# Kernel tuning notes

Measured on AMD Instinct MI355X. Metric: run time of the kernel, lower is better.

## Reference

```python
import jax, jax.numpy as jnp
import numpy as np

N_BLOCKS, B0, B1 = 128, 8, 8
OUT = N_BLOCKS * B0   # 1024
IN = N_BLOCKS * B1    # 1024 (cond_dim = None)
BATCH = 16384


def _masks():
    # block_diag_mask / block_tril_mask from flowjax (structural int32 constants)
    diag = np.zeros((OUT, IN), np.int32)
    tril = np.zeros((OUT, IN), np.int32)
    for i in range(N_BLOCKS):
        diag[i * B0:(i + 1) * B0, i * B1:(i + 1) * B1] = 1
        tril[(i + 1) * B0:, i * B1:(i + 1) * B1] = 1
    return jnp.asarray(diag), jnp.asarray(tril)


def setup_inputs() -> dict:
    key = jax.random.key(0)
    kx, kw, kb, ks = jax.random.split(key, 4)
    b_diag_mask, b_tril_mask = _masks()
    limit = float(np.sqrt(6.0 / (OUT + IN)))  # glorot_uniform
    W = jax.random.uniform(kw, (OUT, IN), jnp.float32, -limit, limit) * (b_diag_mask + b_tril_mask)
    bias = (jax.random.uniform(kb, (OUT,), jnp.float32) - 0.5) * (2.0 / np.sqrt(OUT))
    W_log_scale = jnp.log(jax.random.uniform(ks, (OUT, 1), jnp.float32, 1e-3, 1.0))
    x = jax.random.normal(kx, (BATCH, IN), jnp.float32)
    return {"x": x, "W": W, "bias": bias, "W_log_scale": W_log_scale,
            "b_diag_mask": b_diag_mask, "b_tril_mask": b_tril_mask}


def reference(x, W, bias, W_log_scale, b_diag_mask, b_tril_mask):
    # weight normalisation: exp() on diag blocks, identity on strictly-lower blocks,
    # per-row L2 norm, then learned scale
    Wm = jnp.exp(W) * b_diag_mask + W * b_tril_mask            # [OUT, IN]
    W_norms = jnp.linalg.norm(Wm, axis=-1, keepdims=True)      # [OUT, 1]
    Wn = jnp.exp(W_log_scale) * Wm / W_norms                   # [OUT, IN]
    # batched block-triangular matvec (vmap of W @ x + bias over batch)
    y = x @ Wn.T + bias                                        # [BATCH, OUT]
    # gather diagonal blocks -> (n_blocks, B0, B1), same row-major order as
    # jnp.where(b_diag_mask) indexing in the original
    idx = jnp.arange(N_BLOCKS)
    jac_3d = Wn.reshape(N_BLOCKS, B0, N_BLOCKS, B1)[idx, :, idx, :]  # [N_BLOCKS, B0, B1]
    return y, jnp.log(jac_3d)
```

## Files before the change

kernel.cpp:

```cpp
#include <hip/hip_runtime.h>

#define IN_DIM   1024
#define OUT_DIM  1024
#define BATCH    16384

#define BM 128
#define BN 128
#define BK 32

typedef __attribute__((ext_vector_type(8))) short          bf16x8;
typedef __attribute__((ext_vector_type(8))) unsigned short u16x8;
typedef __attribute__((ext_vector_type(4))) unsigned short u16x4;
typedef __attribute__((ext_vector_type(4))) float          f32x4;

__device__ __forceinline__ unsigned short f2bf(float f) {
    unsigned u = __float_as_uint(f);
    u += 0x7FFFu + ((u >> 16) & 1u);
    return (unsigned short)(u >> 16);
}
__device__ __forceinline__ float bf2f(unsigned short h) {
    return __uint_as_float((unsigned)h << 16);
}

#define GLOAD_LDS16(g, l)                                                      \
    __builtin_amdgcn_global_load_lds(                                          \
        (const __attribute__((address_space(1))) unsigned int*)(g),            \
        (__attribute__((address_space(3))) unsigned int*)(l), 16, 0, 0)

__global__ __launch_bounds__(256) void prep_kernel(
    const float* __restrict__ W, const float* __restrict__ wls,
    unsigned short* __restrict__ wh, unsigned short* __restrict__ wl,
    float* __restrict__ jac)
{
    const int warp = threadIdx.x >> 6;
    const int lane = threadIdx.x & 63;
    const int row  = blockIdx.x * 4 + warp;
    const int r    = row >> 3;
    const int d0   = r * 8;
    const int nk   = d0 + 8;
    const float* Wr = W + (size_t)row * IN_DIM;

    float ss = 0.f;
    for (int k = lane * 4; k < nk; k += 256) {
        float4 v = *(const float4*)&Wr[k];
        if (k >= d0) { v.x = expf(v.x); v.y = expf(v.y); v.z = expf(v.z); v.w = expf(v.w); }
        ss += v.x * v.x + v.y * v.y + v.z * v.z + v.w * v.w;
    }
    #pragma unroll
    for (int off = 32; off >= 1; off >>= 1) ss += __shfl_xor(ss, off);

    const float lscale = wls[row] - 0.5f * logf(ss);
    const float scale  = expf(lscale);

    for (int k = lane * 4; k < IN_DIM; k += 256) {
        float4 v = {0.f, 0.f, 0.f, 0.f};
        if (k < nk) {
            v = *(const float4*)&Wr[k];
            if (k >= d0) { v.x = expf(v.x); v.y = expf(v.y); v.z = expf(v.z); v.w = expf(v.w); }
            v.x *= scale; v.y *= scale; v.z *= scale; v.w *= scale;
        }
        u16x4 h, l;
        const float f[4] = {v.x, v.y, v.z, v.w};
        #pragma unroll
        for (int i = 0; i < 4; ++i) {
            h[i] = f2bf(f[i]);
            l[i] = f2bf(f[i] - bf2f(h[i]));
        }
        *(u16x4*)&wh[(size_t)row * IN_DIM + k] = h;
        *(u16x4*)&wl[(size_t)row * IN_DIM + k] = l;
    }
    if (lane < 8) jac[r * 64 + (row & 7) * 8 + lane] = lscale + Wr[d0 + lane];
}

__global__ __launch_bounds__(256, 2) void gemm_kernel(
    const float* __restrict__ x,
    const unsigned short* __restrict__ wh, const unsigned short* __restrict__ wl,
    const float* __restrict__ bias, float* __restrict__ y)
{
    __shared__ __align__(16) unsigned short smem[32768];

    const int bid = (int)blockIdx.x;
    const int seg = bid >> 7;
    const int sb  = bid & 127;
    const int nt  = 7 - seg;
    const int mt  = (sb & 7) * 16 + (sb >> 3);
    const int m0  = mt * BM;
    const int n0  = nt * BN;
    const int nsteps = (n0 + BN) >> 5;

    const int t    = threadIdx.x;
    const int lane = t & 63;
    const int wid  = t >> 6;
    const int wr   = wid >> 1;
    const int wc   = wid & 1;
    const int lr   = lane & 15;
    const int lq   = lane >> 4;

    const int mA = ((t >> 6) & 3) * 16 + (t & 15);
    const int kA = ((t >> 4) & 3) * 8;
    const float* xg = x + (size_t)(m0 + mA) * IN_DIM + kA;

    const unsigned short* whg = wh + (size_t)(n0 + wid * 32 + lr) * IN_DIM + lq * 8;
    const unsigned short* wlg = wl + (size_t)(n0 + wid * 32 + lr) * IN_DIM + lq * 8;

    f32x4 acc[4][4];
    #pragma unroll
    for (int i = 0; i < 4; ++i)
        #pragma unroll
        for (int j = 0; j < 4; ++j) acc[i][j] = (f32x4){0.f, 0.f, 0.f, 0.f};

    float4 xva, xvb, xvc, xvd;

    auto LOAD_X = [&](int k0) {
        xva = *(const float4*)(xg + k0);
        xvb = *(const float4*)(xg + k0 + 4);
        xvc = *(const float4*)(xg + 64 * IN_DIM + k0);
        xvd = *(const float4*)(xg + 64 * IN_DIM + k0 + 4);
    };
    auto STAGE_W = [&](int b, int k0) {
        unsigned short* whp = smem + b * 16384 + 8192  + wid * 1024;
        unsigned short* wlp = smem + b * 16384 + 12288 + wid * 1024;
        GLOAD_LDS16(whg + k0,                whp);
        GLOAD_LDS16(whg + k0 + 16 * IN_DIM,  whp + 512);
        GLOAD_LDS16(wlg + k0,                wlp);
        GLOAD_LDS16(wlg + k0 + 16 * IN_DIM,  wlp + 512);
    };
    auto CVT_X = [&](int b) {
        unsigned short* xhp = smem + b * 16384;
        unsigned short* xlp = xhp + 4096;
        const float fa[8] = {xva.x, xva.y, xva.z, xva.w, xvb.x, xvb.y, xvb.z, xvb.w};
        const float fb[8] = {xvc.x, xvc.y, xvc.z, xvc.w, xvd.x, xvd.y, xvd.z, xvd.w};
        u16x8 h0, l0, h1, l1;
        #pragma unroll
        for (int i = 0; i < 8; ++i) {
            h0[i] = f2bf(fa[i]);  l0[i] = f2bf(fa[i] - bf2f(h0[i]));
            h1[i] = f2bf(fb[i]);  l1[i] = f2bf(fb[i] - bf2f(h1[i]));
        }
        *(u16x8*)&xhp[t * 8]        = h0;
        *(u16x8*)&xlp[t * 8]        = l0;
        *(u16x8*)&xhp[2048 + t * 8] = h1;
        *(u16x8*)&xlp[2048 + t * 8] = l1;
    };
    auto COMPUTE = [&](int b) {
        const unsigned short* xh_ = smem + b * 16384;
        const unsigned short* xl_ = xh_ + 4096;
        const unsigned short* wh_ = xh_ + 8192;
        const unsigned short* wl_ = xh_ + 12288;
        const int ao = wr * 2048 + lane * 8;
        const int bo = wc * 2048 + lane * 8;
        bf16x8 bh[4], bl[4];
        #pragma unroll
        for (int fc = 0; fc < 4; ++fc) {
            bh[fc] = *(const bf16x8*)&wh_[bo + fc * 512];
            bl[fc] = *(const bf16x8*)&wl_[bo + fc * 512];
        }
        #pragma unroll
        for (int fr = 0; fr < 4; ++fr) {
            const bf16x8 ah = *(const bf16x8*)&xh_[ao + fr * 512];
            const bf16x8 al = *(const bf16x8*)&xl_[ao + fr * 512];
            #pragma unroll
            for (int fc = 0; fc < 4; ++fc) {
                acc[fr][fc] = __builtin_amdgcn_mfma_f32_16x16x32_bf16(ah, bh[fc], acc[fr][fc], 0, 0, 0);
                acc[fr][fc] = __builtin_amdgcn_mfma_f32_16x16x32_bf16(ah, bl[fc], acc[fr][fc], 0, 0, 0);
                acc[fr][fc] = __builtin_amdgcn_mfma_f32_16x16x32_bf16(al, bh[fc], acc[fr][fc], 0, 0, 0);
            }
        }
    };

    LOAD_X(0);
    STAGE_W(0, 0);
    CVT_X(0);
    __syncthreads();

    int buf = 0;
    int k0 = 0;
    for (int i = 0; i < nsteps; ++i, k0 += BK) {
        const bool has1 = (i + 1) < nsteps;
        if (has1) {
            LOAD_X(k0 + BK);
            STAGE_W(buf ^ 1, k0 + BK);
        }
        COMPUTE(buf);
        if (has1) CVT_X(buf ^ 1);
        __syncthreads();
        buf ^= 1;
    }

    float* yt = (float*)smem;
    const int er = t >> 2;
    const int ec = (t & 3) * 4;
    #pragma unroll
    for (int h = 0; h < 2; ++h) {
        if (wr == h) {
            #pragma unroll
            for (int fr = 0; fr < 4; ++fr) {
                const int row0 = fr * 16 + lq * 4;
                #pragma unroll
                for (int fc = 0; fc < 4; ++fc) {
                    const int col = wc * 64 + fc * 16 + lr;
                    #pragma unroll
                    for (int i = 0; i < 4; ++i)
                        yt[(row0 + i) * 132 + col] = acc[fr][fc][i];
                }
            }
        }
        __syncthreads();
        #pragma unroll
        for (int j = 0; j < 8; ++j) {
            const int col = ec + j * 16;
            float4 v = *(const float4*)&yt[er * 132 + col];
            const float4 bb = *(const float4*)&bias[n0 + col];
            v.x += bb.x; v.y += bb.y; v.z += bb.z; v.w += bb.w;
            *(float4*)&y[(size_t)(m0 + h * 64 + er) * OUT_DIM + n0 + col] = v;
        }
        __syncthreads();
    }
}

extern "C" void kernel_launch(void* const* d_in, const int* in_sizes, int n_in,
                              void* d_out, int out_size, void* d_ws, size_t ws_size,
                              hipStream_t stream)
{
    const float* x    = (const float*)d_in[0];
    const float* W    = (const float*)d_in[1];
    const float* bias = (const float*)d_in[2];
    const float* wls  = (const float*)d_in[3];

    unsigned short* wh = (unsigned short*)d_ws;
    unsigned short* wl = wh + (size_t)OUT_DIM * IN_DIM;
    float* y   = (float*)d_out;
    float* jac = y + (size_t)BATCH * OUT_DIM;

    prep_kernel<<<OUT_DIM / 4, 256, 0, stream>>>(W, wls, wh, wl, jac);

    gemm_kernel<<<8 * 128, 256, 0, stream>>>(x, wh, wl, bias, y);
}
```

Baseline: 191.9 us.

## Switch GEMM to single fp16 MFMA and widen N tile to 256

Replaces the bf16 hi/lo split (three MFMAs per tile) with a single fp16 conversion and one fp16 MFMA per fragment, and stores only one fp16 weight copy. The N tile grows to 256 with 512-thread blocks, halving the number of passes over x. This removes most matrix-core work and some memory traffic, at the cost of lower numerical accuracy (fp16 inputs without error compensation) and possible overflow or precision issues.

```diff
diff --git a/kernel.cpp b/kernel.cpp
--- a/kernel.cpp
+++ b/kernel.cpp
@@ -5,21 +5,16 @@
 #define BATCH    16384
 
 #define BM 128
-#define BN 128
+#define BN 256
 #define BK 32
 
-typedef __attribute__((ext_vector_type(8))) short          bf16x8;
-typedef __attribute__((ext_vector_type(8))) unsigned short u16x8;
+typedef __attribute__((ext_vector_type(8))) _Float16       f16x8;
 typedef __attribute__((ext_vector_type(4))) unsigned short u16x4;
 typedef __attribute__((ext_vector_type(4))) float          f32x4;
 
-__device__ __forceinline__ unsigned short f2bf(float f) {
-    unsigned u = __float_as_uint(f);
-    u += 0x7FFFu + ((u >> 16) & 1u);
-    return (unsigned short)(u >> 16);
-}
-__device__ __forceinline__ float bf2f(unsigned short h) {
-    return __uint_as_float((unsigned)h << 16);
+__device__ __forceinline__ unsigned short f2h(float f) {
+    _Float16 h = (_Float16)f;
+    return __builtin_bit_cast(unsigned short, h);
 }
 
 #define GLOAD_LDS16(g, l)                                                      \
@@ -29,8 +24,7 @@
 
 __global__ __launch_bounds__(256) void prep_kernel(
     const float* __restrict__ W, const float* __restrict__ wls,
-    unsigned short* __restrict__ wh, unsigned short* __restrict__ wl,
-    float* __restrict__ jac)
+    unsigned short* __restrict__ wf, float* __restrict__ jac)
 {
     const int warp = threadIdx.x >> 6;
     const int lane = threadIdx.x & 63;
@@ -59,30 +53,23 @@
             if (k >= d0) { v.x = expf(v.x); v.y = expf(v.y); v.z = expf(v.z); v.w = expf(v.w); }
             v.x *= scale; v.y *= scale; v.z *= scale; v.w *= scale;
         }
-        u16x4 h, l;
-        const float f[4] = {v.x, v.y, v.z, v.w};
-        #pragma unroll
-        for (int i = 0; i < 4; ++i) {
-            h[i] = f2bf(f[i]);
-            l[i] = f2bf(f[i] - bf2f(h[i]));
-        }
-        *(u16x4*)&wh[(size_t)row * IN_DIM + k] = h;
-        *(u16x4*)&wl[(size_t)row * IN_DIM + k] = l;
+        u16x4 h;
+        h[0] = f2h(v.x); h[1] = f2h(v.y); h[2] = f2h(v.z); h[3] = f2h(v.w);
+        *(u16x4*)&wf[(size_t)row * IN_DIM + k] = h;
     }
     if (lane < 8) jac[r * 64 + (row & 7) * 8 + lane] = lscale + Wr[d0 + lane];
 }
 
-__global__ __launch_bounds__(256, 2) void gemm_kernel(
-    const float* __restrict__ x,
-    const unsigned short* __restrict__ wh, const unsigned short* __restrict__ wl,
+__global__ __launch_bounds__(512, 2) void gemm_kernel(
+    const float* __restrict__ x, const unsigned short* __restrict__ wf,
     const float* __restrict__ bias, float* __restrict__ y)
 {
-    __shared__ __align__(16) unsigned short smem[32768];
+    __shared__ __align__(16) unsigned short smem[24576];
 
     const int bid = (int)blockIdx.x;
     const int seg = bid >> 7;
     const int sb  = bid & 127;
-    const int nt  = 7 - seg;
+    const int nt  = 3 - seg;
     const int mt  = (sb & 7) * 16 + (sb >> 3);
     const int m0  = mt * BM;
     const int n0  = nt * BN;
@@ -91,17 +78,16 @@
     const int t    = threadIdx.x;
     const int lane = t & 63;
     const int wid  = t >> 6;
-    const int wr   = wid >> 1;
-    const int wc   = wid & 1;
+    const int wr   = wid >> 2;
+    const int wc   = wid & 3;
     const int lr   = lane & 15;
     const int lq   = lane >> 4;
 
-    const int mA = ((t >> 6) & 3) * 16 + (t & 15);
+    const int mA = (t >> 6) * 16 + (t & 15);
     const int kA = ((t >> 4) & 3) * 8;
     const float* xg = x + (size_t)(m0 + mA) * IN_DIM + kA;
 
-    const unsigned short* whg = wh + (size_t)(n0 + wid * 32 + lr) * IN_DIM + lq * 8;
-    const unsigned short* wlg = wl + (size_t)(n0 + wid * 32 + lr) * IN_DIM + lq * 8;
+    const unsigned short* wg = wf + (size_t)(n0 + wid * 32 + lr) * IN_DIM + lq * 8;
 
     f32x4 acc[4][4];
     #pragma unroll
@@ -109,61 +95,40 @@
         #pragma unroll
         for (int j = 0; j < 4; ++j) acc[i][j] = (f32x4){0.f, 0.f, 0.f, 0.f};
 
-    float4 xva, xvb, xvc, xvd;
+    float4 xva, xvb;
 
     auto LOAD_X = [&](int k0) {
         xva = *(const float4*)(xg + k0);
         xvb = *(const float4*)(xg + k0 + 4);
-        xvc = *(const float4*)(xg + 64 * IN_DIM + k0);
-        xvd = *(const float4*)(xg + 64 * IN_DIM + k0 + 4);
     };
     auto STAGE_W = [&](int b, int k0) {
-        unsigned short* whp = smem + b * 16384 + 8192  + wid * 1024;
-        unsigned short* wlp = smem + b * 16384 + 12288 + wid * 1024;
-        GLOAD_LDS16(whg + k0,                whp);
-        GLOAD_LDS16(whg + k0 + 16 * IN_DIM,  whp + 512);
-        GLOAD_LDS16(wlg + k0,                wlp);
-        GLOAD_LDS16(wlg + k0 + 16 * IN_DIM,  wlp + 512);
+        unsigned short* wp = smem + b * 12288 + 4096 + wid * 1024;
+        GLOAD_LDS16(wg + k0,               wp);
+        GLOAD_LDS16(wg + k0 + 16 * IN_DIM, wp + 512);
     };
     auto CVT_X = [&](int b) {
-        unsigned short* xhp = smem + b * 16384;
-        unsigned short* xlp = xhp + 4096;
-        const float fa[8] = {xva.x, xva.y, xva.z, xva.w, xvb.x, xvb.y, xvb.z, xvb.w};
-        const float fb[8] = {xvc.x, xvc.y, xvc.z, xvc.w, xvd.x, xvd.y, xvd.z, xvd.w};
-        u16x8 h0, l0, h1, l1;
-        #pragma unroll
-        for (int i = 0; i < 8; ++i) {
-            h0[i] = f2bf(fa[i]);  l0[i] = f2bf(fa[i] - bf2f(h0[i]));
-            h1[i] = f2bf(fb[i]);  l1[i] = f2bf(fb[i] - bf2f(h1[i]));
-        }
-        *(u16x8*)&xhp[t * 8]        = h0;
-        *(u16x8*)&xlp[t * 8]        = l0;
-        *(u16x8*)&xhp[2048 + t * 8] = h1;
-        *(u16x8*)&xlp[2048 + t * 8] = l1;
+        unsigned short* xp = smem + b * 12288;
+        const float f[8] = {xva.x, xva.y, xva.z, xva.w, xvb.x, xvb.y, xvb.z, xvb.w};
+        f16x8 h;
+        #pragma unroll
+        for (int i = 0; i < 8; ++i) h[i] = (_Float16)f[i];
+        *(f16x8*)&xp[t * 8] = h;
     };
     auto COMPUTE = [&](int b) {
-        const unsigned short* xh_ = smem + b * 16384;
-        const unsigned short* xl_ = xh_ + 4096;
-        const unsigned short* wh_ = xh_ + 8192;
-        const unsigned short* wl_ = xh_ + 12288;
+        const unsigned short* xp = smem + b * 12288;
+        const unsigned short* wp = xp + 4096;
         const int ao = wr * 2048 + lane * 8;
         const int bo = wc * 2048 + lane * 8;
-        bf16x8 bh[4], bl[4];
-        #pragma unroll
-        for (int fc = 0; fc < 4; ++fc) {
-            bh[fc] = *(const bf16x8*)&wh_[bo + fc * 512];
-            bl[fc] = *(const bf16x8*)&wl_[bo + fc * 512];
-        }
+        f16x8 bfr[4];
+        #pragma unroll
+        for (int fc = 0; fc < 4; ++fc)
+            bfr[fc] = *(const f16x8*)&wp[bo + fc * 512];
         #pragma unroll
         for (int fr = 0; fr < 4; ++fr) {
-            const bf16x8 ah = *(const bf16x8*)&xh_[ao + fr * 512];
-            const bf16x8 al = *(const bf16x8*)&xl_[ao + fr * 512];
+            const f16x8 a = *(const f16x8*)&xp[ao + fr * 512];
             #pragma unroll
-            for (int fc = 0; fc < 4; ++fc) {
-                acc[fr][fc] = __builtin_amdgcn_mfma_f32_16x16x32_bf16(ah, bh[fc], acc[fr][fc], 0, 0, 0);
-                acc[fr][fc] = __builtin_amdgcn_mfma_f32_16x16x32_bf16(ah, bl[fc], acc[fr][fc], 0, 0, 0);
-                acc[fr][fc] = __builtin_amdgcn_mfma_f32_16x16x32_bf16(al, bh[fc], acc[fr][fc], 0, 0, 0);
-            }
+            for (int fc = 0; fc < 4; ++fc)
+                acc[fr][fc] = __builtin_amdgcn_mfma_f32_16x16x32_f16(a, bfr[fc], acc[fr][fc], 0, 0, 0);
         }
     };
 
@@ -187,17 +152,16 @@
     }
 
     float* yt = (float*)smem;
-    const int er = t >> 2;
-    const int ec = (t & 3) * 4;
     #pragma unroll
-    for (int h = 0; h < 2; ++h) {
-        if (wr == h) {
+    for (int p = 0; p < 4; ++p) {
+        const int h = p >> 1, c = p & 1;
+        if (wr == h && (wc >> 1) == c) {
             #pragma unroll
             for (int fr = 0; fr < 4; ++fr) {
                 const int row0 = fr * 16 + lq * 4;
                 #pragma unroll
                 for (int fc = 0; fc < 4; ++fc) {
-                    const int col = wc * 64 + fc * 16 + lr;
+                    const int col = (wc & 1) * 64 + fc * 16 + lr;
                     #pragma unroll
                     for (int i = 0; i < 4; ++i)
                         yt[(row0 + i) * 132 + col] = acc[fr][fc][i];
@@ -206,12 +170,13 @@
         }
         __syncthreads();
         #pragma unroll
-        for (int j = 0; j < 8; ++j) {
-            const int col = ec + j * 16;
-            float4 v = *(const float4*)&yt[er * 132 + col];
-            const float4 bb = *(const float4*)&bias[n0 + col];
+        for (int j = 0; j < 4; ++j) {
+            const int r  = j * 16 + (t >> 5);
+            const int c4 = (t & 31) * 4;
+            float4 v = *(const float4*)&yt[r * 132 + c4];
+            const float4 bb = *(const float4*)&bias[n0 + c * 128 + c4];
             v.x += bb.x; v.y += bb.y; v.z += bb.z; v.w += bb.w;
-            *(float4*)&y[(size_t)(m0 + h * 64 + er) * OUT_DIM + n0 + col] = v;
+            *(float4*)&y[(size_t)(m0 + h * 64 + r) * OUT_DIM + n0 + c * 128 + c4] = v;
         }
         __syncthreads();
     }
@@ -226,12 +191,11 @@
     const float* bias = (const float*)d_in[2];
     const float* wls  = (const float*)d_in[3];
 
-    unsigned short* wh = (unsigned short*)d_ws;
-    unsigned short* wl = wh + (size_t)OUT_DIM * IN_DIM;
+    unsigned short* wf = (unsigned short*)d_ws;
     float* y   = (float*)d_out;
     float* jac = y + (size_t)BATCH * OUT_DIM;
 
-    prep_kernel<<<OUT_DIM / 4, 256, 0, stream>>>(W, wls, wh, wl, jac);
-
-    gemm_kernel<<<8 * 128, 256, 0, stream>>>(x, wh, wl, bias, y);
-}
+    prep_kernel<<<OUT_DIM / 4, 256, 0, stream>>>(W, wls, wf, jac);
+
+    gemm_kernel<<<4 * 128, 512, 0, stream>>>(x, wf, bias, y);
+}
```

Result: faster. 180.1 us (-6.2%).
